# Kernel tuning notes

Measured on AMD Instinct MI355X. Metric: run time of the kernel, lower is better.

## Reference

```python
import jax, jax.numpy as jnp
import numpy as np

B, T, LQ, LC = 8, 256, 20, 10
DIM, H = 128, 8
VDIM, WDIM, CDIM = 1024, 300, 50
WORDS, CHARS = 10000, 100


def _build_edges(T, B):
    """Replicates build_graph_edges(hops=2) + build_semantic_edges + build_query_edges,
    then expand_edge_index_for_batch with num_nodes = T + 1.  Static numpy (jit-safe)."""
    N = T + 1
    es = []
    for h in (1, 2):  # temporal edges, 2 hops (indices replicate original code exactly)
        i = np.arange(T - h)
        es += [np.stack([i, i + h]), np.stack([i + h, i])]
    i = np.arange(T)  # query<->segment edges inside build_graph_edges
    z = np.zeros(T, dtype=np.int64)
    es += [np.stack([z, i + 1]), np.stack([i + 1, z])]
    temporal = np.concatenate(es, axis=1)
    a, b = np.triu_indices(T, k=1)  # torch.combinations(arange(T), r=2)
    sem = np.concatenate([np.stack([a, b]), np.stack([b, a])], axis=1)
    qe = np.stack([np.concatenate([[0], np.arange(1, T + 1)]),
                   np.concatenate([np.arange(1, T + 1), [0]])])
    off = (np.arange(B, dtype=np.int64) * N)[None, :, None]
    expand = lambda e: (e[:, None, :].astype(np.int64) + off).reshape(2, -1)
    return np.concatenate([expand(temporal), expand(sem), expand(qe)], axis=1)


def setup_inputs() -> dict:
    key = jax.random.key(0)
    ks = jax.random.split(key, 16)
    w = lambda k, shape: jax.random.normal(k, shape, jnp.float32) * 0.02
    return {
        "word_ids": jax.random.randint(ks[0], (B, LQ), 0, WORDS),
        "char_ids": jax.random.randint(ks[1], (B, LQ, LC), 0, CHARS),
        "video_features": jax.random.normal(ks[2], (B, T, VDIM), jnp.float32),
        "v_mask": jnp.ones((B, T), jnp.float32),
        "q_mask": jnp.ones((B, LQ), jnp.float32),
        "word_emb": w(ks[3], (WORDS, WDIM)),
        "char_emb": w(ks[4], (CHARS, CDIM)),
        "W_embed": w(ks[5], (WDIM + CDIM, DIM)), "b_embed": jnp.zeros((DIM,), jnp.float32),
        "W_vproj": w(ks[6], (VDIM, DIM)), "b_vproj": jnp.zeros((DIM,), jnp.float32),
        "W_enc": w(ks[7], (DIM, DIM)), "b_enc": jnp.zeros((DIM,), jnp.float32),
        "Wq": w(ks[8], (DIM, DIM)), "bq": jnp.zeros((DIM,), jnp.float32),
        "Wk": w(ks[9], (DIM, DIM)), "bk": jnp.zeros((DIM,), jnp.float32),
        "Wv": w(ks[10], (DIM, DIM)), "bv": jnp.zeros((DIM,), jnp.float32),
        "Wskip": w(ks[11], (DIM, DIM)), "bskip": jnp.zeros((DIM,), jnp.float32),
        "W_start": w(ks[12], (DIM, 1)), "b_start": jnp.zeros((1,), jnp.float32),
        "W_end": w(ks[13], (DIM, 1)), "b_end": jnp.zeros((1,), jnp.float32),
    }


def reference(word_ids, char_ids, video_features, v_mask, q_mask,
              word_emb, char_emb, W_embed, b_embed, W_vproj, b_vproj,
              W_enc, b_enc, Wq, bq, Wk, bk, Wv, bv, Wskip, bskip,
              W_start, b_start, W_end, b_end):
    enc = lambda x, m: jax.nn.relu(x @ W_enc + b_enc) * m[..., None]  # shared feature encoder (stand-in)
    # video branch
    vfeat = enc(video_features @ W_vproj + b_vproj, v_mask)            # [B, T, DIM]
    # query branch: word + char embeddings -> dim, encode, mean-pool
    qemb = jnp.concatenate([word_emb[word_ids], char_emb[char_ids].mean(axis=2)], axis=-1)
    qfeat = enc(qemb @ W_embed + b_embed, q_mask).mean(axis=1)         # [B, DIM]
    nodes = jnp.concatenate([qfeat[:, None, :], vfeat], axis=1)        # [B, N, DIM], N = T+1
    Bn, N, _ = nodes.shape
    Nn = Bn * N
    xf = nodes.reshape(Nn, DIM)
    edges = jnp.asarray(_build_edges(N - 1, Bn))                       # [2, E] static
    src, dst = edges[0], edges[1]                                      # PyG: messages x_j=src -> target i=dst
    hd = DIM // H
    q = (xf @ Wq + bq).reshape(Nn, H, hd)
    k = (xf @ Wk + bk).reshape(Nn, H, hd)
    v = (xf @ Wv + bv).reshape(Nn, H, hd)
    # TransformerConv: per-edge attention logits, segment-softmax over incoming edges
    logits = (q[dst] * k[src]).sum(-1) / float(np.sqrt(hd))            # [E, H]
    mx = jax.ops.segment_max(logits, dst, num_segments=Nn)
    ex = jnp.exp(logits - mx[dst])
    den = jax.ops.segment_sum(ex, dst, num_segments=Nn)
    alpha = ex / (den[dst] + 1e-16)
    agg = jax.ops.segment_sum(alpha[:, :, None] * v[src], dst, num_segments=Nn)  # [Nn, H, hd]
    out = agg.reshape(Nn, DIM) + xf @ Wskip + bskip                    # root_weight skip connection
    out = out.reshape(Bn, N, DIM)
    start_logits = (out[:, 1:] @ W_start + b_start)[..., 0]            # [B, T]
    end_logits = (out[:, 1:] @ W_end + b_end)[..., 0]                  # [B, T]
    return start_logits, end_logits
```

## Files before the change

kernel.cpp:

```cpp
#include <hip/hip_runtime.h>
#include <hip/hip_bf16.h>
#include <math.h>

#define B_ 8
#define T_ 256
#define LQ_ 20
#define LC_ 10
#define DIM_ 128
#define N_ 257
#define NN_ (B_*N_)

#define FMA4(a, s, ww) { (a).x += (s)*(ww).x; (a).y += (s)*(ww).y; (a).z += (s)*(ww).z; (a).w += (s)*(ww).w; }

typedef __attribute__((ext_vector_type(8))) short bf16x8;
typedef __attribute__((ext_vector_type(4))) float f32x4;

__device__ __forceinline__ unsigned short f2bf(float f) {
  unsigned u = __float_as_uint(f);
  unsigned r = u + 0x7FFFu + ((u >> 16) & 1u);
  return (unsigned short)(r >> 16);
}
__device__ __forceinline__ float bf2f(unsigned short h) {
  return __uint_as_float(((unsigned)h) << 16);
}

__global__ __launch_bounds__(256) void kPRE(
    const int* __restrict__ word_ids, const int* __restrict__ char_ids,
    const float* __restrict__ word_emb, const float* __restrict__ char_emb,
    const float* __restrict__ W_embed, const float* __restrict__ b_embed,
    const float* __restrict__ We, const float* __restrict__ be,
    const float* __restrict__ q_mask,
    const float* __restrict__ Wv,
    float* __restrict__ eq,
    unsigned short* __restrict__ WvTh, unsigned short* __restrict__ WvTl)
{
  __shared__ __align__(16) float smem[2112];
  const int blk = blockIdx.x, tid = threadIdx.x;
  if (blk < 160) {
    const int qi = blk;
    const int b = qi / 20, lq = qi - b * 20;
    float* emb = smem;
    float* ps  = emb + 352;
    float* hq  = emb + 608;
    float* pe  = emb + 736;
    const int wid = word_ids[b * LQ_ + lq];
    for (int m2 = tid; m2 < 300; m2 += 256) emb[m2] = word_emb[(size_t)wid * 300 + m2];
    if (tid < 50) {
      float s = 0.f;
      #pragma unroll
      for (int l = 0; l < 10; ++l) {
        const int cid = char_ids[(b * LQ_ + lq) * 10 + l];
        s += char_emb[cid * 50 + tid];
      }
      emb[300 + tid] = s * 0.1f;
    }
    __syncthreads();
    const int j = tid & 127, half = tid >> 7;
    {
      float a = 0.f;
      const float* Wcol = W_embed + (size_t)(half * 175) * 128 + j;
      const float* eh = emb + half * 175;
      #pragma unroll 5
      for (int m2 = 0; m2 < 175; ++m2) a += eh[m2] * Wcol[(size_t)m2 * 128];
      ps[half * 128 + j] = a;
    }
    __syncthreads();
    if (tid < 128) hq[tid] = ps[tid] + ps[128 + tid] + b_embed[tid];
    __syncthreads();
    {
      float e = 0.f;
      #pragma unroll 8
      for (int kk = 0; kk < 64; ++kk)
        e += hq[half * 64 + kk] * We[(half * 64 + kk) * 128 + j];
      pe[half * 128 + j] = e;
    }
    __syncthreads();
    if (tid < 128) {
      float ev = pe[tid] + pe[128 + tid] + be[tid];
      ev = fmaxf(ev, 0.f) * q_mask[b * LQ_ + lq];
      eq[(size_t)qi * 128 + tid] = ev;
    }
  } else {
    const int k0 = (blk - 160) * 16;
    const float4* src = reinterpret_cast<const float4*>(Wv + (size_t)k0 * 128);
    #pragma unroll
    for (int i = 0; i < 2; ++i) {
      const int idx4 = tid + i * 256;
      const int r = idx4 >> 5, f = idx4 & 31;
      *reinterpret_cast<float4*>(&smem[r * 132 + f * 4]) = src[r * 32 + f];
    }
    __syncthreads();
    const int col = tid & 127, kg = tid >> 7;
    bf16x8 vh, vl;
    #pragma unroll
    for (int j = 0; j < 8; ++j) {
      const int kk = kg * 8 + j;
      const float xv = smem[kk * 132 + col];
      const unsigned short hi = f2bf(xv);
      const unsigned short lo = f2bf(xv - bf2f(hi));
      vh[j] = (short)hi; vl[j] = (short)lo;
    }
    *reinterpret_cast<bf16x8*>(WvTh + (size_t)col * 1024 + k0 + kg * 8) = vh;
    *reinterpret_cast<bf16x8*>(WvTl + (size_t)col * 1024 + k0 + kg * 8) = vl;
  }
}

__global__ __launch_bounds__(512) void kVID(
    const float* __restrict__ video,
    const unsigned short* __restrict__ WvTh,
    const unsigned short* __restrict__ WvTl,
    float* __restrict__ h2)
{
  __shared__ unsigned short Ah[16 * 512];
  __shared__ unsigned short Al[16 * 512];
  const int blk = blockIdx.x, tid = threadIdx.x;
  const int rt = blk >> 1, kh = blk & 1;
  const int r0 = rt * 16;
  #pragma unroll
  for (int i = 0; i < 2; ++i) {
    const int g = tid * 2 + i;
    const int row = g >> 6, gk = g & 63;
    const float* src = video + (size_t)(r0 + row) * 1024 + kh * 512 + gk * 8;
    const float4 x0 = *reinterpret_cast<const float4*>(src);
    const float4 x1 = *reinterpret_cast<const float4*>(src + 4);
    const float xs[8] = {x0.x, x0.y, x0.z, x0.w, x1.x, x1.y, x1.z, x1.w};
    bf16x8 vh, vl;
    #pragma unroll
    for (int j = 0; j < 8; ++j) {
      const unsigned short hi = f2bf(xs[j]);
      const unsigned short lo = f2bf(xs[j] - bf2f(hi));
      vh[j] = (short)hi; vl[j] = (short)lo;
    }
    int byteoff = row * 1024 + gk * 16;
    byteoff ^= ((row & 7) << 4);
    *reinterpret_cast<bf16x8*>(reinterpret_cast<char*>(Ah) + byteoff) = vh;
    *reinterpret_cast<bf16x8*>(reinterpret_cast<char*>(Al) + byteoff) = vl;
  }
  __syncthreads();
  const int wv = tid >> 6, lane = tid & 63;
  const int col16 = lane & 15, kg8 = lane >> 4;
  const int c0 = wv * 16;
  const unsigned short* pBh = WvTh + (size_t)(c0 + col16) * 1024 + kh * 512;
  const unsigned short* pBl = WvTl + (size_t)(c0 + col16) * 1024 + kh * 512;
  const int arow = lane & 15;
  const int abase = arow * 1024;
  f32x4 acc = {0.f, 0.f, 0.f, 0.f};
  #pragma unroll 4
  for (int t = 0; t < 16; ++t) {
    const int kb = t * 32 + kg8 * 8;
    const int aoff = (abase + kb * 2) ^ ((arow & 7) << 4);
    const bf16x8 ah = *reinterpret_cast<const bf16x8*>(reinterpret_cast<const char*>(Ah) + aoff);
    const bf16x8 al = *reinterpret_cast<const bf16x8*>(reinterpret_cast<const char*>(Al) + aoff);
    const bf16x8 bh = *reinterpret_cast<const bf16x8*>(pBh + kb);
    const bf16x8 bl = *reinterpret_cast<const bf16x8*>(pBl + kb);
    acc = __builtin_amdgcn_mfma_f32_16x16x32_bf16(ah, bh, acc, 0, 0, 0);
    acc = __builtin_amdgcn_mfma_f32_16x16x32_bf16(ah, bl, acc, 0, 0, 0);
    acc = __builtin_amdgcn_mfma_f32_16x16x32_bf16(al, bh, acc, 0, 0, 0);
  }
  const int ocol = c0 + col16;
  const int orow = (lane >> 4) * 4;
  float* hdst = h2 + (size_t)kh * 2048 * 128;
  #pragma unroll
  for (int i2 = 0; i2 < 4; ++i2)
    hdst[(size_t)(r0 + orow + i2) * 128 + ocol] = acc[i2];
}

__global__ __launch_bounds__(512) void kMAIN(
    const float* __restrict__ h2, const float* __restrict__ bvp,
    const float* __restrict__ We, const float* __restrict__ be,
    const float* __restrict__ vmask,
    const float* __restrict__ Wq, const float* __restrict__ bq,
    const float* __restrict__ Wk, const float* __restrict__ bk,
    const float* __restrict__ Wvv, const float* __restrict__ bval,
    const float* __restrict__ Ws, const float* __restrict__ bs,
    float* __restrict__ q, float* __restrict__ k,
    float* __restrict__ v, float* __restrict__ sk)
{
  __shared__ __align__(16) float smem_f[19008];
  float4* ps4 = reinterpret_cast<float4*>(smem_f);
  float* hl = smem_f + 16896;
  float* xe = smem_f + 17952;
  const int blk = blockIdx.x, tid = threadIdx.x;
  const float* Wm[4] = {Wq, Wk, Wvv, Ws};
  const float* bm[4] = {bq, bk, bval, bs};
  float* om[4] = {q, k, v, sk};
  const int r0 = blk * 8;
  if (tid < 256) {
    const int r = tid >> 5, c = tid & 31;
    const float4 p0 = *reinterpret_cast<const float4*>(h2 + (size_t)(r0 + r) * 128 + c * 4);
    const float4 p1 = *reinterpret_cast<const float4*>(h2 + (size_t)(2048 + r0 + r) * 128 + c * 4);
    float4 s = reinterpret_cast<const float4*>(bvp)[c];
    s.x += p0.x + p1.x; s.y += p0.y + p1.y;
    s.z += p0.z + p1.z; s.w += p0.w + p1.w;
    *reinterpret_cast<float4*>(&hl[r * 132 + c * 4]) = s;
  }
  __syncthreads();
  const int c4 = tid & 31, ks = tid >> 5;
  float4 acc[8];
  #pragma unroll
  for (int r = 0; r < 8; ++r) acc[r] = float4{0.f, 0.f, 0.f, 0.f};
  {
    const float4* We4 = reinterpret_cast<const float4*>(We) + c4;
    #pragma unroll
    for (int kc = 0; kc < 2; ++kc) {
      const int k0 = ks * 8 + kc * 4;
      const float4 w0 = We4[(size_t)(k0 + 0) * 32];
      const float4 w1 = We4[(size_t)(k0 + 1) * 32];
      const float4 w2 = We4[(size_t)(k0 + 2) * 32];
      const float4 w3 = We4[(size_t)(k0 + 3) * 32];
      #pragma unroll
      for (int r = 0; r < 8; ++r) {
        const float4 rv = *reinterpret_cast<const float4*>(&hl[r * 132 + k0]);
        FMA4(acc[r], rv.x, w0); FMA4(acc[r], rv.y, w1);
        FMA4(acc[r], rv.z, w2); FMA4(acc[r], rv.w, w3);
      }
    }
  }
  #pragma unroll
  for (int r = 0; r < 8; ++r) ps4[(ks * 8 + r) * 33 + c4] = acc[r];
  __syncthreads();
  if (tid < 256) {
    const int r = tid >> 5, c = tid & 31;
    float4 s = reinterpret_cast<const float4*>(be)[c];
    #pragma unroll
    for (int ke = 0; ke < 16; ++ke) {
      const float4 p = ps4[(ke * 8 + r) * 33 + c];
      s.x += p.x; s.y += p.y; s.z += p.z; s.w += p.w;
    }
    const float mk = vmask[r0 + r];
    s.x = fmaxf(s.x, 0.f) * mk; s.y = fmaxf(s.y, 0.f) * mk;
    s.z = fmaxf(s.z, 0.f) * mk; s.w = fmaxf(s.w, 0.f) * mk;
    *reinterpret_cast<float4*>(&xe[r * 132 + c * 4]) = s;
  }
  __syncthreads();
  const int m = ks >> 2, keP = ks & 3;
  #pragma unroll
  for (int r = 0; r < 8; ++r) acc[r] = float4{0.f, 0.f, 0.f, 0.f};
  {
    const float4* Wp4 = reinterpret_cast<const float4*>(Wm[m]) + c4;
    #pragma unroll
    for (int kc = 0; kc < 8; ++kc) {
      const int k0 = keP * 32 + kc * 4;
      const float4 w0 = Wp4[(size_t)(k0 + 0) * 32];
      const float4 w1 = Wp4[(size_t)(k0 + 1) * 32];
      const float4 w2 = Wp4[(size_t)(k0 + 2) * 32];
      const float4 w3 = Wp4[(size_t)(k0 + 3) * 32];
      #pragma unroll
      for (int r = 0; r < 8; ++r) {
        const float4 rv = *reinterpret_cast<const float4*>(&xe[r * 132 + k0]);
        FMA4(acc[r], rv.x, w0); FMA4(acc[r], rv.y, w1);
        FMA4(acc[r], rv.z, w2); FMA4(acc[r], rv.w, w3);
      }
    }
  }
  #pragma unroll
  for (int r = 0; r < 8; ++r) ps4[(ks * 8 + r) * 33 + c4] = acc[r];
  __syncthreads();
  #pragma unroll
  for (int it = 0; it < 2; ++it) {
    const int id = tid + it * 512;
    const int mm = id >> 8, r = (id >> 5) & 7, c = id & 31;
    float4 s = reinterpret_cast<const float4*>(bm[mm])[c];
    #pragma unroll
    for (int ke = 0; ke < 4; ++ke) {
      const float4 p = ps4[((mm * 4 + ke) * 8 + r) * 33 + c];
      s.x += p.x; s.y += p.y; s.z += p.z; s.w += p.w;
    }
    const int vr = r0 + r;
    const int node = (vr >> 8) * 257 + 1 + (vr & 255);
    *reinterpret_cast<float4*>(om[mm] + (size_t)node * 128 + 4 * c) = s;
  }
}

__device__ __forceinline__ float cntf(int dnode, int s) {
  if (dnode == 256) return (s == 0 ? 1.f : 0.f) + (s == 255 ? 1.f : 0.f);
  float c = (s != dnode) ? 1.f : 0.f;
  if (s == 0) c += 1.f;
  if (s == dnode - 1) c += 2.f;
  if (s == dnode + 1 && dnode <= 254) c += 1.f;
  if (s == dnode - 2 && dnode >= 2) c += 1.f;
  if (s == dnode + 2 && dnode <= 253) c += 1.f;
  return c;
}

__global__ __launch_bounds__(256) void kATTN(
    const float* __restrict__ q, const float* __restrict__ k,
    const float* __restrict__ v, const float* __restrict__ eq,
    const float* __restrict__ Wk, const float* __restrict__ bk,
    const float* __restrict__ Wvv, const float* __restrict__ bval,
    float* __restrict__ npart, float* __restrict__ dpart)
{
  __shared__ float Kl[32][128];
  __shared__ float Vl[32][128];
  __shared__ float m0[128];
  const int d0 = blockIdx.x * 32;
  const int y  = blockIdx.y;
  const int b  = blockIdx.z;
  const int tid = threadIdx.x;
  const int base = b * 257;
  const int s0 = y * 32;
  {
    const float4* ksrc = reinterpret_cast<const float4*>(k + (size_t)(base + s0) * 128);
    const float4* vsrc = reinterpret_cast<const float4*>(v + (size_t)(base + s0) * 128);
    float4* kd = reinterpret_cast<float4*>(Kl);
    float4* vd = reinterpret_cast<float4*>(Vl);
    #pragma unroll
    for (int i = 0; i < 4; ++i) {
      kd[tid + i * 256] = ksrc[tid + i * 256];
      vd[tid + i * 256] = vsrc[tid + i * 256];
    }
  }
  if (y == 0 && tid < 128) {
    float s = 0.f;
    #pragma unroll 4
    for (int lq = 0; lq < LQ_; ++lq) s += eq[((size_t)b * LQ_ + lq) * 128 + tid];
    m0[tid] = s * (1.f / LQ_);
  }
  const int dd = tid >> 3, h = tid & 7;
  const int dnode = d0 + dd + 1;
  const float* qrow = q + (size_t)(base + dnode) * 128 + h * 16;
  const float4 qq0 = *(const float4*)(qrow + 0);
  const float4 qq1 = *(const float4*)(qrow + 4);
  const float4 qq2 = *(const float4*)(qrow + 8);
  const float4 qq3 = *(const float4*)(qrow + 12);
  __syncthreads();
  if (y == 0) {
    const int j = tid & 127, half = tid >> 7;
    const float* W = half ? Wvv : Wk;
    float acc = half ? bval[j] : bk[j];
    #pragma unroll 8
    for (int kk = 0; kk < 128; ++kk) acc += m0[kk] * W[kk * 128 + j];
    if (half) Vl[0][j] = acc; else Kl[0][j] = acc;
  }
  __syncthreads();

  float den = 0.f;
  float4 o0 = {0,0,0,0}, o1 = {0,0,0,0}, o2 = {0,0,0,0}, o3 = {0,0,0,0};
  #pragma unroll 2
  for (int s = 0; s < 32; ++s) {
    const float* krow = &Kl[s][h * 16];
    const float4 k0 = *(const float4*)(krow + 0);
    const float4 k1 = *(const float4*)(krow + 4);
    const float4 k2 = *(const float4*)(krow + 8);
    const float4 k3 = *(const float4*)(krow + 12);
    float dt = qq0.x*k0.x + qq0.y*k0.y + qq0.z*k0.z + qq0.w*k0.w
             + qq1.x*k1.x + qq1.y*k1.y + qq1.z*k1.z + qq1.w*k1.w
             + qq2.x*k2.x + qq2.y*k2.y + qq2.z*k2.z + qq2.w*k2.w
             + qq3.x*k3.x + qq3.y*k3.y + qq3.z*k3.z + qq3.w*k3.w;
    const float c = cntf(dnode, s0 + s);
    const float pw = c * __expf(dt * 0.25f);
    den += pw;
    const float* vrow = &Vl[s][h * 16];
    const float4 v0 = *(const float4*)(vrow + 0);
    const float4 v1 = *(const float4*)(vrow + 4);
    const float4 v2 = *(const float4*)(vrow + 8);
    const float4 v3 = *(const float4*)(vrow + 12);
    o0.x += pw*v0.x; o0.y += pw*v0.y; o0.z += pw*v0.z; o0.w += pw*v0.w;
    o1.x += pw*v1.x; o1.y += pw*v1.y; o1.z += pw*v1.z; o1.w += pw*v1.w;
    o2.x += pw*v2.x; o2.y += pw*v2.y; o2.z += pw*v2.z; o2.w += pw*v2.w;
    o3.x += pw*v3.x; o3.y += pw*v3.y; o3.z += pw*v3.z; o3.w += pw*v3.w;
  }
  const size_t pb = ((size_t)y * 8 + b) * 256 + d0;
  float* np = npart + (pb + dd) * 128 + h * 16;
  *reinterpret_cast<float4*>(np + 0)  = o0;
  *reinterpret_cast<float4*>(np + 4)  = o1;
  *reinterpret_cast<float4*>(np + 8)  = o2;
  *reinterpret_cast<float4*>(np + 12) = o3;
  dpart[(pb + dd) * 8 + h] = den;
}

__global__ __launch_bounds__(256) void kRED(
    const float* __restrict__ npart, const float* __restrict__ dpart,
    const float* __restrict__ sk,
    const float* __restrict__ W_start, const float* __restrict__ b_start,
    const float* __restrict__ W_end, const float* __restrict__ b_end,
    float* __restrict__ out)
{
  __shared__ float red[16][2][2];
  const int d0 = blockIdx.x * 16;
  const int b = blockIdx.y;
  const int tid = threadIdx.x;
  const int base = b * 257;
  const int jB = tid & 127, shB = tid >> 7;
  const int hB = jB >> 4;
  const float wst = W_start[jB], wen = W_end[jB];
  #pragma unroll
  for (int dd8 = 0; dd8 < 8; ++dd8) {
    const int dd = shB * 8 + dd8;
    const int dst = d0 + dd;
    float num = 0.f, den = 0.f;
    #pragma unroll
    for (int y = 0; y < 8; ++y) {
      const size_t pb = ((size_t)y * 8 + b) * 256 + dst;
      num += npart[pb * 128 + jB];
      den += dpart[pb * 8 + hB];
    }
    const float o = num / (den + 1e-16f) + sk[(size_t)(base + dst + 1) * 128 + jB];
    float psum = o * wst, pesum = o * wen;
    #pragma unroll
    for (int off = 1; off < 64; off <<= 1) {
      psum += __shfl_xor(psum, off);
      pesum += __shfl_xor(pesum, off);
    }
    if ((tid & 63) == 0) { red[dd][jB >> 6][0] = psum; red[dd][jB >> 6][1] = pesum; }
  }
  __syncthreads();
  if (tid < 16) {
    out[b * 256 + d0 + tid]        = red[tid][0][0] + red[tid][1][0] + b_start[0];
    out[2048 + b * 256 + d0 + tid] = red[tid][0][1] + red[tid][1][1] + b_end[0];
  }
}

extern "C" void kernel_launch(void* const* d_in, const int* in_sizes, int n_in,
                              void* d_out, int out_size, void* d_ws, size_t ws_size,
                              hipStream_t stream) {
  const int*   word_ids = (const int*)d_in[0];
  const int*   char_ids = (const int*)d_in[1];
  const float* video    = (const float*)d_in[2];
  const float* v_mask   = (const float*)d_in[3];
  const float* q_mask   = (const float*)d_in[4];
  const float* word_emb = (const float*)d_in[5];
  const float* char_emb = (const float*)d_in[6];
  const float* W_embed  = (const float*)d_in[7];
  const float* b_embed  = (const float*)d_in[8];
  const float* W_vproj  = (const float*)d_in[9];
  const float* b_vproj  = (const float*)d_in[10];
  const float* W_enc    = (const float*)d_in[11];
  const float* b_enc    = (const float*)d_in[12];
  const float* Wq       = (const float*)d_in[13];
  const float* bq       = (const float*)d_in[14];
  const float* Wk       = (const float*)d_in[15];
  const float* bk       = (const float*)d_in[16];
  const float* Wv       = (const float*)d_in[17];
  const float* bv       = (const float*)d_in[18];
  const float* Wskip    = (const float*)d_in[19];
  const float* bskip    = (const float*)d_in[20];
  const float* W_start  = (const float*)d_in[21];
  const float* b_start  = (const float*)d_in[22];
  const float* W_end    = (const float*)d_in[23];
  const float* b_end    = (const float*)d_in[24];

  float* q     = (float*)d_ws;
  float* k     = q  + NN_ * DIM_;
  float* v     = k  + NN_ * DIM_;
  float* sk    = v  + NN_ * DIM_;
  float* eq    = sk + NN_ * DIM_;
  float* npart = eq + 160 * 128;
  float* dpart = npart + (size_t)8 * 8 * 256 * 128;
  float* h2    = dpart + 16384;
  unsigned short* WvTh = (unsigned short*)(h2 + (size_t)2 * 2048 * 128);
  unsigned short* WvTl = WvTh + 128 * 1024;

  hipLaunchKernelGGL(kPRE, dim3(224), dim3(256), 0, stream,
    word_ids, char_ids, word_emb, char_emb, W_embed, b_embed,
    W_enc, b_enc, q_mask, W_vproj, eq, WvTh, WvTl);
  hipLaunchKernelGGL(kVID, dim3(256), dim3(512), 0, stream,
    video, WvTh, WvTl, h2);
  hipLaunchKernelGGL(kMAIN, dim3(256), dim3(512), 0, stream,
    h2, b_vproj, W_enc, b_enc, v_mask,
    Wq, bq, Wk, bk, Wv, bv, Wskip, bskip, q, k, v, sk);
  hipLaunchKernelGGL(kATTN, dim3(8, 8, 8), dim3(256), 0, stream,
    q, k, v, eq, Wk, bk, Wv, bv, npart, dpart);
  hipLaunchKernelGGL(kRED, dim3(16, 8), dim3(256), 0, stream,
    npart, dpart, sk, W_start, b_start, W_end, b_end, (float*)d_out);
}
```

Baseline: 65.49 us.

## Fuse video projection, encoder and QKV/skip projections into one MFMA kernel

Merges the separate video-projection (split-K) kernel and the fp32 FMA encoder/QKV kernel into a single kernel. Each block handles 16 rows across the full K=1024 and chains the encoder and four projection GEMMs through LDS using split-bf16 MFMA. The encoder and projection weights are pre-converted to transposed hi/lo bf16 in kPRE. This removes one launch and the h2 global round-trip, and moves the small GEMMs onto matrix cores. The cost is only 128 blocks, each doing the whole K loop, which lowers parallelism for the large GEMM.

```diff
diff --git a/kernel.cpp b/kernel.cpp
--- a/kernel.cpp
+++ b/kernel.cpp
@@ -10,8 +10,6 @@
 #define N_ 257
 #define NN_ (B_*N_)
 
-#define FMA4(a, s, ww) { (a).x += (s)*(ww).x; (a).y += (s)*(ww).y; (a).z += (s)*(ww).z; (a).w += (s)*(ww).w; }
-
 typedef __attribute__((ext_vector_type(8))) short bf16x8;
 typedef __attribute__((ext_vector_type(4))) float f32x4;
 
@@ -31,8 +29,11 @@
     const float* __restrict__ We, const float* __restrict__ be,
     const float* __restrict__ q_mask,
     const float* __restrict__ Wv,
+    const float* __restrict__ Wq, const float* __restrict__ Wk,
+    const float* __restrict__ Wvv, const float* __restrict__ Ws,
     float* __restrict__ eq,
-    unsigned short* __restrict__ WvTh, unsigned short* __restrict__ WvTl)
+    unsigned short* __restrict__ WvTh, unsigned short* __restrict__ WvTl,
+    unsigned short* __restrict__ WcH, unsigned short* __restrict__ WcL)
 {
   __shared__ __align__(16) float smem[2112];
   const int blk = blockIdx.x, tid = threadIdx.x;
@@ -81,13 +82,23 @@
       eq[(size_t)qi * 128 + tid] = ev;
     }
   } else {
-    const int k0 = (blk - 160) * 16;
-    const float4* src = reinterpret_cast<const float4*>(Wv + (size_t)k0 * 128);
+    const float* src; unsigned short *dh, *dl; int k0, KD;
+    int cb = blk - 160;
+    if (cb < 64) { k0 = cb * 16; KD = 1024; src = Wv + (size_t)k0 * 128; dh = WvTh; dl = WvTl; }
+    else {
+      cb -= 64;
+      const int m = cb >> 3, kr = cb & 7;
+      const float* Wmat[5] = {We, Wq, Wk, Wvv, Ws};
+      k0 = kr * 16; KD = 128;
+      src = Wmat[m] + (size_t)k0 * 128;
+      dh = WcH + (size_t)m * 16384; dl = WcL + (size_t)m * 16384;
+    }
+    const float4* s4 = reinterpret_cast<const float4*>(src);
     #pragma unroll
     for (int i = 0; i < 2; ++i) {
       const int idx4 = tid + i * 256;
       const int r = idx4 >> 5, f = idx4 & 31;
-      *reinterpret_cast<float4*>(&smem[r * 132 + f * 4]) = src[r * 32 + f];
+      *reinterpret_cast<float4*>(&smem[r * 132 + f * 4]) = s4[r * 32 + f];
     }
     __syncthreads();
     const int col = tid & 127, kg = tid >> 7;
@@ -100,27 +111,37 @@
       const unsigned short lo = f2bf(xv - bf2f(hi));
       vh[j] = (short)hi; vl[j] = (short)lo;
     }
-    *reinterpret_cast<bf16x8*>(WvTh + (size_t)col * 1024 + k0 + kg * 8) = vh;
-    *reinterpret_cast<bf16x8*>(WvTl + (size_t)col * 1024 + k0 + kg * 8) = vl;
-  }
-}
-
-__global__ __launch_bounds__(512) void kVID(
+    *reinterpret_cast<bf16x8*>(dh + (size_t)col * KD + k0 + kg * 8) = vh;
+    *reinterpret_cast<bf16x8*>(dl + (size_t)col * KD + k0 + kg * 8) = vl;
+  }
+}
+
+__global__ __launch_bounds__(512) void kNMF(
     const float* __restrict__ video,
-    const unsigned short* __restrict__ WvTh,
-    const unsigned short* __restrict__ WvTl,
-    float* __restrict__ h2)
+    const unsigned short* __restrict__ WvTh, const unsigned short* __restrict__ WvTl,
+    const unsigned short* __restrict__ WcH, const unsigned short* __restrict__ WcL,
+    const float* __restrict__ bvp, const float* __restrict__ be,
+    const float* __restrict__ vmask,
+    const float* __restrict__ bq, const float* __restrict__ bk,
+    const float* __restrict__ bval, const float* __restrict__ bs,
+    float* __restrict__ q, float* __restrict__ k,
+    float* __restrict__ v, float* __restrict__ sk)
 {
-  __shared__ unsigned short Ah[16 * 512];
-  __shared__ unsigned short Al[16 * 512];
+  __shared__ __align__(16) unsigned short Abuf[32 * 1024];
+  char* Ahb = reinterpret_cast<char*>(Abuf);
+  char* Alb = Ahb + 32768;
+  float* hl = reinterpret_cast<float*>(Abuf);
+  float* xe = hl + 2112;
   const int blk = blockIdx.x, tid = threadIdx.x;
-  const int rt = blk >> 1, kh = blk & 1;
-  const int r0 = rt * 16;
+  const int r0 = blk * 16;
+  const float* bm[4] = {bq, bk, bval, bs};
+  float* om[4] = {q, k, v, sk};
+
   #pragma unroll
-  for (int i = 0; i < 2; ++i) {
-    const int g = tid * 2 + i;
-    const int row = g >> 6, gk = g & 63;
-    const float* src = video + (size_t)(r0 + row) * 1024 + kh * 512 + gk * 8;
+  for (int i = 0; i < 4; ++i) {
+    const int g = i * 512 + tid;
+    const int row = g >> 7, gk = g & 127;
+    const float* src = video + (size_t)(r0 + row) * 1024 + gk * 8;
     const float4 x0 = *reinterpret_cast<const float4*>(src);
     const float4 x1 = *reinterpret_cast<const float4*>(src + 4);
     const float xs[8] = {x0.x, x0.y, x0.z, x0.w, x1.x, x1.y, x1.z, x1.w};
@@ -131,144 +152,124 @@
       const unsigned short lo = f2bf(xs[j] - bf2f(hi));
       vh[j] = (short)hi; vl[j] = (short)lo;
     }
-    int byteoff = row * 1024 + gk * 16;
-    byteoff ^= ((row & 7) << 4);
-    *reinterpret_cast<bf16x8*>(reinterpret_cast<char*>(Ah) + byteoff) = vh;
-    *reinterpret_cast<bf16x8*>(reinterpret_cast<char*>(Al) + byteoff) = vl;
-  }
-  __syncthreads();
+    const int byteoff = (row * 2048 + gk * 16) ^ ((row & 7) << 4);
+    *reinterpret_cast<bf16x8*>(Ahb + byteoff) = vh;
+    *reinterpret_cast<bf16x8*>(Alb + byteoff) = vl;
+  }
+  __syncthreads();
+
   const int wv = tid >> 6, lane = tid & 63;
   const int col16 = lane & 15, kg8 = lane >> 4;
   const int c0 = wv * 16;
-  const unsigned short* pBh = WvTh + (size_t)(c0 + col16) * 1024 + kh * 512;
-  const unsigned short* pBl = WvTl + (size_t)(c0 + col16) * 1024 + kh * 512;
   const int arow = lane & 15;
-  const int abase = arow * 1024;
-  f32x4 acc = {0.f, 0.f, 0.f, 0.f};
-  #pragma unroll 4
-  for (int t = 0; t < 16; ++t) {
-    const int kb = t * 32 + kg8 * 8;
-    const int aoff = (abase + kb * 2) ^ ((arow & 7) << 4);
-    const bf16x8 ah = *reinterpret_cast<const bf16x8*>(reinterpret_cast<const char*>(Ah) + aoff);
-    const bf16x8 al = *reinterpret_cast<const bf16x8*>(reinterpret_cast<const char*>(Al) + aoff);
-    const bf16x8 bh = *reinterpret_cast<const bf16x8*>(pBh + kb);
-    const bf16x8 bl = *reinterpret_cast<const bf16x8*>(pBl + kb);
-    acc = __builtin_amdgcn_mfma_f32_16x16x32_bf16(ah, bh, acc, 0, 0, 0);
-    acc = __builtin_amdgcn_mfma_f32_16x16x32_bf16(ah, bl, acc, 0, 0, 0);
-    acc = __builtin_amdgcn_mfma_f32_16x16x32_bf16(al, bh, acc, 0, 0, 0);
-  }
   const int ocol = c0 + col16;
   const int orow = (lane >> 4) * 4;
-  float* hdst = h2 + (size_t)kh * 2048 * 128;
+
+  f32x4 acc = {0.f, 0.f, 0.f, 0.f};
+  {
+    const unsigned short* pBh = WvTh + (size_t)ocol * 1024;
+    const unsigned short* pBl = WvTl + (size_t)ocol * 1024;
+    #pragma unroll 4
+    for (int t = 0; t < 32; ++t) {
+      const int kb = t * 32 + kg8 * 8;
+      const int aoff = (arow * 2048 + kb * 2) ^ ((arow & 7) << 4);
+      const bf16x8 ah = *reinterpret_cast<const bf16x8*>(Ahb + aoff);
+      const bf16x8 al = *reinterpret_cast<const bf16x8*>(Alb + aoff);
+      const bf16x8 bh = *reinterpret_cast<const bf16x8*>(pBh + kb);
+      const bf16x8 bl = *reinterpret_cast<const bf16x8*>(pBl + kb);
+      acc = __builtin_amdgcn_mfma_f32_16x16x32_bf16(ah, bh, acc, 0, 0, 0);
+      acc = __builtin_amdgcn_mfma_f32_16x16x32_bf16(ah, bl, acc, 0, 0, 0);
+      acc = __builtin_amdgcn_mfma_f32_16x16x32_bf16(al, bh, acc, 0, 0, 0);
+    }
+  }
+  __syncthreads();
+  {
+    const float bv = bvp[ocol];
+    #pragma unroll
+    for (int i = 0; i < 4; ++i) hl[(orow + i) * 132 + ocol] = acc[i] + bv;
+  }
+  __syncthreads();
+
+  bf16x8 ahE[4], alE[4];
   #pragma unroll
-  for (int i2 = 0; i2 < 4; ++i2)
-    hdst[(size_t)(r0 + orow + i2) * 128 + ocol] = acc[i2];
-}
-
-__global__ __launch_bounds__(512) void kMAIN(
-    const float* __restrict__ h2, const float* __restrict__ bvp,
-    const float* __restrict__ We, const float* __restrict__ be,
-    const float* __restrict__ vmask,
-    const float* __restrict__ Wq, const float* __restrict__ bq,
-    const float* __restrict__ Wk, const float* __restrict__ bk,
-    const float* __restrict__ Wvv, const float* __restrict__ bval,
-    const float* __restrict__ Ws, const float* __restrict__ bs,
-    float* __restrict__ q, float* __restrict__ k,
-    float* __restrict__ v, float* __restrict__ sk)
-{
-  __shared__ __align__(16) float smem_f[19008];
-  float4* ps4 = reinterpret_cast<float4*>(smem_f);
-  float* hl = smem_f + 16896;
-  float* xe = smem_f + 17952;
-  const int blk = blockIdx.x, tid = threadIdx.x;
-  const float* Wm[4] = {Wq, Wk, Wvv, Ws};
-  const float* bm[4] = {bq, bk, bval, bs};
-  float* om[4] = {q, k, v, sk};
-  const int r0 = blk * 8;
-  if (tid < 256) {
-    const int r = tid >> 5, c = tid & 31;
-    const float4 p0 = *reinterpret_cast<const float4*>(h2 + (size_t)(r0 + r) * 128 + c * 4);
-    const float4 p1 = *reinterpret_cast<const float4*>(h2 + (size_t)(2048 + r0 + r) * 128 + c * 4);
-    float4 s = reinterpret_cast<const float4*>(bvp)[c];
-    s.x += p0.x + p1.x; s.y += p0.y + p1.y;
-    s.z += p0.z + p1.z; s.w += p0.w + p1.w;
-    *reinterpret_cast<float4*>(&hl[r * 132 + c * 4]) = s;
-  }
-  __syncthreads();
-  const int c4 = tid & 31, ks = tid >> 5;
-  float4 acc[8];
+  for (int t = 0; t < 4; ++t) {
+    const int kbase = t * 32 + kg8 * 8;
+    const float4 f0 = *reinterpret_cast<const float4*>(&hl[arow * 132 + kbase]);
+    const float4 f1 = *reinterpret_cast<const float4*>(&hl[arow * 132 + kbase + 4]);
+    const float fs[8] = {f0.x, f0.y, f0.z, f0.w, f1.x, f1.y, f1.z, f1.w};
+    #pragma unroll
+    for (int j = 0; j < 8; ++j) {
+      const unsigned short hi = f2bf(fs[j]);
+      const unsigned short lo = f2bf(fs[j] - bf2f(hi));
+      ahE[t][j] = (short)hi; alE[t][j] = (short)lo;
+    }
+  }
+  acc = f32x4{0.f, 0.f, 0.f, 0.f};
+  {
+    const unsigned short* pBh = WcH + (size_t)ocol * 128;
+    const unsigned short* pBl = WcL + (size_t)ocol * 128;
+    #pragma unroll
+    for (int t = 0; t < 4; ++t) {
+      const int kb = t * 32 + kg8 * 8;
+      const bf16x8 bh = *reinterpret_cast<const bf16x8*>(pBh + kb);
+      const bf16x8 bl = *reinterpret_cast<const bf16x8*>(pBl + kb);
+      acc = __builtin_amdgcn_mfma_f32_16x16x32_bf16(ahE[t], bh, acc, 0, 0, 0);
+      acc = __builtin_amdgcn_mfma_f32_16x16x32_bf16(ahE[t], bl, acc, 0, 0, 0);
+      acc = __builtin_amdgcn_mfma_f32_16x16x32_bf16(alE[t], bh, acc, 0, 0, 0);
+    }
+  }
+  __syncthreads();
+  {
+    const float bev = be[ocol];
+    #pragma unroll
+    for (int i = 0; i < 4; ++i) {
+      float xv = acc[i] + bev;
+      xv = fmaxf(xv, 0.f) * vmask[r0 + orow + i];
+      xe[(orow + i) * 132 + ocol] = xv;
+    }
+  }
+  __syncthreads();
+
+  const int m = wv >> 1, ch = wv & 1;
+  bf16x8 ahP[4], alP[4];
   #pragma unroll
-  for (int r = 0; r < 8; ++r) acc[r] = float4{0.f, 0.f, 0.f, 0.f};
-  {
-    const float4* We4 = reinterpret_cast<const float4*>(We) + c4;
-    #pragma unroll
-    for (int kc = 0; kc < 2; ++kc) {
-      const int k0 = ks * 8 + kc * 4;
-      const float4 w0 = We4[(size_t)(k0 + 0) * 32];
-      const float4 w1 = We4[(size_t)(k0 + 1) * 32];
-      const float4 w2 = We4[(size_t)(k0 + 2) * 32];
-      const float4 w3 = We4[(size_t)(k0 + 3) * 32];
-      #pragma unroll
-      for (int r = 0; r < 8; ++r) {
-        const float4 rv = *reinterpret_cast<const float4*>(&hl[r * 132 + k0]);
-        FMA4(acc[r], rv.x, w0); FMA4(acc[r], rv.y, w1);
-        FMA4(acc[r], rv.z, w2); FMA4(acc[r], rv.w, w3);
-      }
-    }
-  }
+  for (int t = 0; t < 4; ++t) {
+    const int kbase = t * 32 + kg8 * 8;
+    const float4 f0 = *reinterpret_cast<const float4*>(&xe[arow * 132 + kbase]);
+    const float4 f1 = *reinterpret_cast<const float4*>(&xe[arow * 132 + kbase + 4]);
+    const float fs[8] = {f0.x, f0.y, f0.z, f0.w, f1.x, f1.y, f1.z, f1.w};
+    #pragma unroll
+    for (int j = 0; j < 8; ++j) {
+      const unsigned short hi = f2bf(fs[j]);
+      const unsigned short lo = f2bf(fs[j] - bf2f(hi));
+      ahP[t][j] = (short)hi; alP[t][j] = (short)lo;
+    }
+  }
+  const unsigned short* WmH = WcH + (size_t)(1 + m) * 16384;
+  const unsigned short* WmL = WcL + (size_t)(1 + m) * 16384;
   #pragma unroll
-  for (int r = 0; r < 8; ++r) ps4[(ks * 8 + r) * 33 + c4] = acc[r];
-  __syncthreads();
-  if (tid < 256) {
-    const int r = tid >> 5, c = tid & 31;
-    float4 s = reinterpret_cast<const float4*>(be)[c];
-    #pragma unroll
-    for (int ke = 0; ke < 16; ++ke) {
-      const float4 p = ps4[(ke * 8 + r) * 33 + c];
-      s.x += p.x; s.y += p.y; s.z += p.z; s.w += p.w;
-    }
-    const float mk = vmask[r0 + r];
-    s.x = fmaxf(s.x, 0.f) * mk; s.y = fmaxf(s.y, 0.f) * mk;
-    s.z = fmaxf(s.z, 0.f) * mk; s.w = fmaxf(s.w, 0.f) * mk;
-    *reinterpret_cast<float4*>(&xe[r * 132 + c * 4]) = s;
-  }
-  __syncthreads();
-  const int m = ks >> 2, keP = ks & 3;
-  #pragma unroll
-  for (int r = 0; r < 8; ++r) acc[r] = float4{0.f, 0.f, 0.f, 0.f};
-  {
-    const float4* Wp4 = reinterpret_cast<const float4*>(Wm[m]) + c4;
-    #pragma unroll
-    for (int kc = 0; kc < 8; ++kc) {
-      const int k0 = keP * 32 + kc * 4;
-      const float4 w0 = Wp4[(size_t)(k0 + 0) * 32];
-      const float4 w1 = Wp4[(size_t)(k0 + 1) * 32];
-      const float4 w2 = Wp4[(size_t)(k0 + 2) * 32];
-      const float4 w3 = Wp4[(size_t)(k0 + 3) * 32];
-      #pragma unroll
-      for (int r = 0; r < 8; ++r) {
-        const float4 rv = *reinterpret_cast<const float4*>(&xe[r * 132 + k0]);
-        FMA4(acc[r], rv.x, w0); FMA4(acc[r], rv.y, w1);
-        FMA4(acc[r], rv.z, w2); FMA4(acc[r], rv.w, w3);
-      }
-    }
-  }
-  #pragma unroll
-  for (int r = 0; r < 8; ++r) ps4[(ks * 8 + r) * 33 + c4] = acc[r];
-  __syncthreads();
-  #pragma unroll
-  for (int it = 0; it < 2; ++it) {
-    const int id = tid + it * 512;
-    const int mm = id >> 8, r = (id >> 5) & 7, c = id & 31;
-    float4 s = reinterpret_cast<const float4*>(bm[mm])[c];
-    #pragma unroll
-    for (int ke = 0; ke < 4; ++ke) {
-      const float4 p = ps4[((mm * 4 + ke) * 8 + r) * 33 + c];
-      s.x += p.x; s.y += p.y; s.z += p.z; s.w += p.w;
-    }
-    const int vr = r0 + r;
-    const int node = (vr >> 8) * 257 + 1 + (vr & 255);
-    *reinterpret_cast<float4*>(om[mm] + (size_t)node * 128 + 4 * c) = s;
+  for (int tt = 0; tt < 4; ++tt) {
+    const int cc0 = ch * 64 + tt * 16;
+    const int occ = cc0 + col16;
+    const unsigned short* pBh = WmH + (size_t)occ * 128;
+    const unsigned short* pBl = WmL + (size_t)occ * 128;
+    f32x4 ac2 = {0.f, 0.f, 0.f, 0.f};
+    #pragma unroll
+    for (int t = 0; t < 4; ++t) {
+      const int kb = t * 32 + kg8 * 8;
+      const bf16x8 bh = *reinterpret_cast<const bf16x8*>(pBh + kb);
+      const bf16x8 bl = *reinterpret_cast<const bf16x8*>(pBl + kb);
+      ac2 = __builtin_amdgcn_mfma_f32_16x16x32_bf16(ahP[t], bh, ac2, 0, 0, 0);
+      ac2 = __builtin_amdgcn_mfma_f32_16x16x32_bf16(ahP[t], bl, ac2, 0, 0, 0);
+      ac2 = __builtin_amdgcn_mfma_f32_16x16x32_bf16(alP[t], bh, ac2, 0, 0, 0);
+    }
+    const float bb = bm[m][occ];
+    #pragma unroll
+    for (int i = 0; i < 4; ++i) {
+      const int vr = r0 + orow + i;
+      const int node = (vr >> 8) * 257 + 1 + (vr & 255);
+      om[m][(size_t)node * 128 + occ] = ac2[i] + bb;
+    }
   }
 }
 
@@ -447,18 +448,18 @@
   float* eq    = sk + NN_ * DIM_;
   float* npart = eq + 160 * 128;
   float* dpart = npart + (size_t)8 * 8 * 256 * 128;
-  float* h2    = dpart + 16384;
-  unsigned short* WvTh = (unsigned short*)(h2 + (size_t)2 * 2048 * 128);
-  unsigned short* WvTl = WvTh + 128 * 1024;
-
-  hipLaunchKernelGGL(kPRE, dim3(224), dim3(256), 0, stream,
+  unsigned short* WvTh = (unsigned short*)(dpart + 16384);
+  unsigned short* WvTl = WvTh + 131072;
+  unsigned short* WcH  = WvTl + 131072;
+  unsigned short* WcL  = WcH + 5 * 16384;
+
+  hipLaunchKernelGGL(kPRE, dim3(264), dim3(256), 0, stream,
     word_ids, char_ids, word_emb, char_emb, W_embed, b_embed,
-    W_enc, b_enc, q_mask, W_vproj, eq, WvTh, WvTl);
-  hipLaunchKernelGGL(kVID, dim3(256), dim3(512), 0, stream,
-    video, WvTh, WvTl, h2);
-  hipLaunchKernelGGL(kMAIN, dim3(256), dim3(512), 0, stream,
-    h2, b_vproj, W_enc, b_enc, v_mask,
-    Wq, bq, Wk, bk, Wv, bv, Wskip, bskip, q, k, v, sk);
+    W_enc, b_enc, q_mask, W_vproj, Wq, Wk, Wv, Wskip,
+    eq, WvTh, WvTl, WcH, WcL);
+  hipLaunchKernelGGL(kNMF, dim3(128), dim3(512), 0, stream,
+    video, WvTh, WvTl, WcH, WcL, b_vproj, b_enc, v_mask,
+    bq, bk, bv, bskip, q, k, v, sk);
   hipLaunchKernelGGL(kATTN, dim3(8, 8, 8), dim3(256), 0, stream,
     q, k, v, eq, Wk, bk, Wv, bv, npart, dpart);
   hipLaunchKernelGGL(kRED, dim3(16, 8), dim3(256), 0, stream,
```

After: 75.88 us. 1.16x slower.
